# Kernel optimization log

Measured on AMD Instinct MI355X. Metric: run time of the kernel, lower is better.

Reference implementation:

```python
import jax, jax.numpy as jnp
import numpy as np

K = 9          # top-k neighbors
GROUPS = 4     # GroupNorm groups
EPS_GN = 1e-5  # torch GroupNorm default eps


def group_norm(x, gamma, beta):
    # x: [B, C, H, W]; normalize over (C/GROUPS, H, W) per group
    B, C, H, W = x.shape
    xg = x.reshape(B, GROUPS, -1)
    mu = xg.mean(axis=-1, keepdims=True)
    var = xg.var(axis=-1, keepdims=True)
    xn = ((xg - mu) / jnp.sqrt(var + EPS_GN)).reshape(B, C, H, W)
    return xn * gamma[None, :, None, None] + beta[None, :, None, None]


def setup_inputs() -> dict:
    key = jax.random.key(0)
    ks = jax.random.split(key, 6)
    B, C, H, W = 32, 128, 45, 45
    std = 1.0 / np.sqrt(C)
    x = jax.random.normal(ks[0], (B, C, H, W), dtype=jnp.float32)
    w1 = jax.random.uniform(ks[1], (C, C), jnp.float32, -std, std)
    b1 = jax.random.uniform(ks[2], (C,), jnp.float32, -std, std)
    w2 = jax.random.uniform(ks[3], (C, C), jnp.float32, -std, std)
    b2 = jax.random.uniform(ks[4], (C,), jnp.float32, -std, std)
    gamma1 = jnp.ones((C,), jnp.float32)
    beta1 = jnp.zeros((C,), jnp.float32)
    gamma2 = jnp.ones((C,), jnp.float32)
    beta2 = jnp.zeros((C,), jnp.float32)
    return {"x": x, "w1": w1, "b1": b1, "w2": w2, "b2": b2,
            "gamma1": gamma1, "beta1": beta1, "gamma2": gamma2, "beta2": beta2}


def reference(x, w1, b1, w2, b2, gamma1, beta1, gamma2, beta2):
    B, C, H, W = x.shape
    N = H * W
    # build_knn: flatten, L2-normalize, cosine sim, top-k
    xf = x.reshape(B, C, N).transpose(0, 2, 1)                  # [B, N, C]
    nrm = jnp.linalg.norm(xf, axis=-1, keepdims=True)
    xn = xf / jnp.maximum(nrm, 1e-12)                           # F.normalize
    sim = jnp.einsum('bnc,bmc->bnm', xn, xn)                    # [B, N, N]
    val, idx = jax.lax.top_k(sim, K)                            # [B, N, K]
    # normalized edge weights (shared by both GCN layers)
    v = val / (val.sum(axis=-1, keepdims=True) + 1e-6)          # [B, N, K]

    def gcn_apply(feat, w, b):
        xt = feat @ w                                           # [B, N, C]
        neigh = jax.vmap(lambda t, i: t[i])(xt, idx)            # [B, N, K, C]
        return jnp.einsum('bnkc,bnk->bnc', neigh, v) + b

    out = gcn_apply(xn, w1, b1)
    out = jax.nn.silu(group_norm(out.transpose(0, 2, 1).reshape(B, C, H, W), gamma1, beta1))
    of = out.reshape(B, C, N).transpose(0, 2, 1)
    out = gcn_apply(of, w2, b2)
    out = jax.nn.silu(group_norm(out.transpose(0, 2, 1).reshape(B, C, H, W), gamma2, beta2))
    return out
```

## Files before the change

kernel.cpp:

```cpp
#include <hip/hip_runtime.h>
#include <hip/hip_bf16.h>

#define BN 32
#define CC 128
#define NN 2025
#define KK 9
#define NGROUP 4
#define CPG 32
#define GN_EPS 1e-5f
#define ROWS_TOTAL (BN * NN)

typedef _Float16 f16;
typedef __attribute__((ext_vector_type(8))) _Float16 f16x8;
typedef __attribute__((ext_vector_type(4))) float f32x4;

#define S28 3.725290298461914e-09f
#define S40 9.094947017729282e-13f
#define RH  6.103515625e-05f
#define RL  1.4901161193847656e-08f

#define T0F 0.17f
#define CAP 100

__global__ __launch_bounds__(256) void k_normalize(const float* __restrict__ x,
                                                   f16* __restrict__ xh, f16* __restrict__ xl) {
    __shared__ float tile[128][65];
    const int b  = blockIdx.y;
    const int n0 = blockIdx.x * 64;
    const int t  = threadIdx.x;
    const int w  = t >> 6;
    const int lane = t & 63;
    const int gn_ld = min(n0 + lane, NN - 1);

    for (int it = 0; it < 32; ++it) {
        int c = it * 4 + w;
        tile[c][lane] = x[((size_t)(b * CC + c)) * NN + gn_ld];
    }
    __syncthreads();

    for (int i = 0; i < 16; ++i) {
        int n  = w * 16 + i;
        int gn = n0 + n;
        if (gn < NN) {
            float v0 = tile[lane][n];
            float v1 = tile[lane + 64][n];
            float ss = v0 * v0 + v1 * v1;
#pragma unroll
            for (int off = 32; off > 0; off >>= 1) ss += __shfl_xor(ss, off);
            float s = 1.0f / fmaxf(sqrtf(ss), 1e-12f);
            v0 *= s; v1 *= s;
            float w0 = v0 * 16384.0f, w1 = v1 * 16384.0f;
            f16 h0 = (f16)w0, h1 = (f16)w1;
            f16 l0 = (f16)((w0 - (float)h0) * 4096.0f);
            f16 l1 = (f16)((w1 - (float)h1) * 4096.0f);
            size_t base = (size_t)(b * NN + gn) * CC;
            xh[base + lane] = h0;  xh[base + lane + 64] = h1;
            xl[base + lane] = l0;  xl[base + lane + 64] = l1;
        }
    }
}

__device__ __forceinline__ void ins9(float cand, int m, float* v, int* ix,
                                     float& mv, int& mi, int& mp) {
    bool take = (cand > mv) || ((cand == mv) && (m < mi));
    if (take) {
#pragma unroll
        for (int k = 0; k < 9; ++k) if (k == mp) { v[k] = cand; ix[k] = m; }
        float nv = v[0]; int ni = ix[0]; int np = 0;
#pragma unroll
        for (int k = 1; k < 9; ++k) {
            if (v[k] < nv || (v[k] == nv && ix[k] > ni)) { nv = v[k]; ni = ix[k]; np = k; }
        }
        mv = nv; mi = ni; mp = np;
    }
}

__global__ __launch_bounds__(256) void k_sim_topk(const f16* __restrict__ xh, const f16* __restrict__ xl,
                                                  float* __restrict__ vout, int* __restrict__ iout) {
    __shared__ f16x8          stg[2][32][16];
    __shared__ float          sv[32][CAP + 1];
    __shared__ unsigned short si[32][CAP + 2];
    __shared__ int   cnt[32];
    __shared__ int   nbad;
    __shared__ int   badrows[32];

    const int id   = blockIdx.x;
    const int b    = (id & 7) + 8 * (id >> 9);
    const int r0   = ((id >> 3) & 63) * 32;
    const int t    = threadIdx.x;
    const int w    = t >> 6;
    const int lane = t & 63;
    const int jr   = lane & 15;
    const int q    = lane >> 4;
    const int tw   = w & 1;
    const int mh   = w >> 1;

    if (t < 32) cnt[t] = 0;
    if (t == 0) nbad = 0;

    f16x8 bh[4], bl[4];
    {
        int rr = b * NN + min(r0 + tw * 16 + jr, NN - 1);
        const f16* pH = xh + (size_t)rr * CC;
        const f16* pL = xl + (size_t)rr * CC;
#pragma unroll
        for (int s = 0; s < 4; ++s) {
            bh[s] = *(const f16x8*)(pH + s * 32 + q * 8);
            bl[s] = *(const f16x8*)(pL + s * 32 + q * 8);
        }
    }

    const int fi_ = t & 15;
    const int ri_ = t >> 4;
    const int fx  = fi_ ^ (ri_ & 7);
    const int rbuf = tw * 16 + jr;

    f16x8 h0r, h1r, l0r, l1r;
    {
        size_t g0 = (size_t)(b * NN + min(ri_, NN - 1)) * CC + fi_ * 8;
        size_t g1 = (size_t)(b * NN + min(ri_ + 16, NN - 1)) * CC + fi_ * 8;
        h0r = *(const f16x8*)(xh + g0);  h1r = *(const f16x8*)(xh + g1);
        l0r = *(const f16x8*)(xl + g0);  l1r = *(const f16x8*)(xl + g1);
    }

    for (int chunk = 0; chunk < 64; ++chunk) {
        __syncthreads();
        stg[0][ri_][fx]      = h0r;
        stg[0][ri_ + 16][fx] = h1r;
        stg[1][ri_][fx]      = l0r;
        stg[1][ri_ + 16][fx] = l1r;
        __syncthreads();
        if (chunk < 63) {
            size_t g0 = (size_t)(b * NN + min((chunk + 1) * 32 + ri_, NN - 1)) * CC + fi_ * 8;
            size_t g1 = (size_t)(b * NN + min((chunk + 1) * 32 + ri_ + 16, NN - 1)) * CC + fi_ * 8;
            h0r = *(const f16x8*)(xh + g0);  h1r = *(const f16x8*)(xh + g1);
            l0r = *(const f16x8*)(xl + g0);  l1r = *(const f16x8*)(xl + g1);
        }
        __builtin_amdgcn_sched_barrier(0);

        const int mb   = chunk * 32 + mh * 16;
        const int arow = mh * 16 + jr;
        const int axr  = arow & 7;
        f32x4 hh = {0.f, 0.f, 0.f, 0.f}, ll = {0.f, 0.f, 0.f, 0.f};
#pragma unroll
        for (int s = 0; s < 4; ++s) {
            f16x8 ah = stg[0][arow][(s * 4 + q) ^ axr];
            f16x8 al = stg[1][arow][(s * 4 + q) ^ axr];
            hh = __builtin_amdgcn_mfma_f32_16x16x32_f16(ah, bh[s], hh, 0, 0, 0);
            ll = __builtin_amdgcn_mfma_f32_16x16x32_f16(ah, bl[s], ll, 0, 0, 0);
            ll = __builtin_amdgcn_mfma_f32_16x16x32_f16(al, bh[s], ll, 0, 0, 0);
        }
#pragma unroll
        for (int reg = 0; reg < 4; ++reg) {
            int m = mb + q * 4 + reg;
            float c0 = hh[reg] * S28 + ll[reg] * S40;
            if (m < NN && c0 > T0F) {
                int pos = atomicAdd(&cnt[rbuf], 1);
                if (pos < CAP) { sv[rbuf][pos] = c0; si[rbuf][pos] = (unsigned short)m; }
            }
        }
    }
    __syncthreads();

    if (t < 32) {
        int r = r0 + t;
        if (r < NN) {
            int c = cnt[t];
            if (c >= 9 && c <= CAP) {
                float fv[9]; int fi[9];
#pragma unroll
                for (int k = 0; k < 9; ++k) { fv[k] = -3.0e38f; fi[k] = 0x7fffffff; }
                float mv = -3.0e38f; int mi = 0x7fffffff; int mp = 0;
                for (int j = 0; j < c; ++j) ins9(sv[t][j], (int)si[t][j], fv, fi, mv, mi, mp);
                float s = 1e-6f;
#pragma unroll
                for (int k = 0; k < 9; ++k) s += fv[k];
                float inv = 1.0f / s;
                int base = (b * NN + r) * KK;
#pragma unroll
                for (int k = 0; k < 9; ++k) { vout[base + k] = fv[k] * inv; iout[base + k] = fi[k]; }
            } else {
                int slot = atomicAdd(&nbad, 1);
                badrows[slot] = r;
            }
        }
    }
    __syncthreads();

    if (w == 0) {
        int nb = nbad;
        for (int ib = 0; ib < nb; ++ib) {
            int r = badrows[ib];
            const f16* rH = xh + ((size_t)b * NN + r) * CC;
            const f16* rL = xl + ((size_t)b * NN + r) * CC;
            float fv[9]; int fi[9];
#pragma unroll
            for (int k = 0; k < 9; ++k) { fv[k] = -3.0e38f; fi[k] = 0x7fffffff; }
            float mv = -3.0e38f; int mi = 0x7fffffff; int mp = 0;
            for (int m = lane; m < NN; m += 64) {
                const f16* mH = xh + ((size_t)b * NN + m) * CC;
                const f16* mL = xl + ((size_t)b * NN + m) * CC;
                float a1 = 0.f, a2 = 0.f;
                for (int c2 = 0; c2 < CC; ++c2) {
                    float hr = (float)rH[c2], hm = (float)mH[c2];
                    float lr = (float)rL[c2], lm = (float)mL[c2];
                    a1 += hr * hm;
                    a2 += hr * lm + lr * hm;
                }
                ins9(a1 * S28 + a2 * S40, m, fv, fi, mv, mi, mp);
            }
#pragma unroll
            for (int off = 1; off < 64; off <<= 1) {
                float pv[9]; int pi[9];
#pragma unroll
                for (int k = 0; k < 9; ++k) { pv[k] = __shfl_xor(fv[k], off); pi[k] = __shfl_xor(fi[k], off); }
#pragma unroll
                for (int k = 0; k < 9; ++k) ins9(pv[k], pi[k], fv, fi, mv, mi, mp);
            }
            if (lane == 0) {
                float s = 1e-6f;
#pragma unroll
                for (int k = 0; k < 9; ++k) s += fv[k];
                float inv = 1.0f / s;
                int base = (b * NN + r) * KK;
#pragma unroll
                for (int k = 0; k < 9; ++k) { vout[base + k] = fv[k] * inv; iout[base + k] = fi[k]; }
            }
        }
    }
}

#define RST 36
__global__ __launch_bounds__(256) void k_gemm_hl(const f16* __restrict__ xh, const f16* __restrict__ xl,
                                                 const float* __restrict__ w, float* __restrict__ out) {
    __shared__ float rowsT[CC * RST];
    int t = threadIdx.x;
    int row0 = blockIdx.x * 32;
    for (int it = 0; it < 16; ++it) {
        int qq = t + it * 256;
        int c = qq & 127, r = qq >> 7;
        size_t idx = (size_t)(row0 + r) * CC + c;
        rowsT[c * RST + r] = (float)xh[idx] * RH + (float)xl[idx] * RL;
    }
    __syncthreads();
    int j = t & 127, half = t >> 7;
    float acc[16];
#pragma unroll
    for (int r = 0; r < 16; ++r) acc[r] = 0.0f;
    for (int c = 0; c < CC; ++c) {
        float wv = w[c * CC + j];
        const float4* ap = (const float4*)&rowsT[c * RST + half * 16];
        float4 a0 = ap[0], a1 = ap[1], a2 = ap[2], a3 = ap[3];
        acc[0]  += a0.x * wv; acc[1]  += a0.y * wv; acc[2]  += a0.z * wv; acc[3]  += a0.w * wv;
        acc[4]  += a1.x * wv; acc[5]  += a1.y * wv; acc[6]  += a1.z * wv; acc[7]  += a1.w * wv;
        acc[8]  += a2.x * wv; acc[9]  += a2.y * wv; acc[10] += a2.z * wv; acc[11] += a2.w * wv;
        acc[12] += a3.x * wv; acc[13] += a3.y * wv; acc[14] += a3.z * wv; acc[15] += a3.w * wv;
    }
#pragma unroll
    for (int r = 0; r < 16; ++r) out[(size_t)(row0 + half * 16 + r) * CC + j] = acc[r];
}

__global__ __launch_bounds__(256) void k_gemm(const float* __restrict__ in,
                                              const float* __restrict__ w,
                                              float* __restrict__ out) {
    __shared__ float rowsT[CC * RST];
    int t = threadIdx.x;
    int row0 = blockIdx.x * 32;
    for (int it = 0; it < 16; ++it) {
        int qq = t + it * 256;
        int c = qq & 127, r = qq >> 7;
        rowsT[c * RST + r] = in[(size_t)(row0 + r) * CC + c];
    }
    __syncthreads();
    int j = t & 127, half = t >> 7;
    float acc[16];
#pragma unroll
    for (int r = 0; r < 16; ++r) acc[r] = 0.0f;
    for (int c = 0; c < CC; ++c) {
        float wv = w[c * CC + j];
        const float4* ap = (const float4*)&rowsT[c * RST + half * 16];
        float4 a0 = ap[0], a1 = ap[1], a2 = ap[2], a3 = ap[3];
        acc[0]  += a0.x * wv; acc[1]  += a0.y * wv; acc[2]  += a0.z * wv; acc[3]  += a0.w * wv;
        acc[4]  += a1.x * wv; acc[5]  += a1.y * wv; acc[6]  += a1.z * wv; acc[7]  += a1.w * wv;
        acc[8]  += a2.x * wv; acc[9]  += a2.y * wv; acc[10] += a2.z * wv; acc[11] += a2.w * wv;
        acc[12] += a3.x * wv; acc[13] += a3.y * wv; acc[14] += a3.z * wv; acc[15] += a3.w * wv;
    }
#pragma unroll
    for (int r = 0; r < 16; ++r) out[(size_t)(row0 + half * 16 + r) * CC + j] = acc[r];
}

__global__ __launch_bounds__(256) void k_gather(const float* __restrict__ xt,
                                                const float* __restrict__ v,
                                                const int* __restrict__ idx,
                                                const float* __restrict__ bias,
                                                float* __restrict__ out) {
    int t = threadIdx.x;
    int g = blockIdx.x * 2 + (t >> 7);
    int c = t & 127;
    if (g >= ROWS_TOTAL) return;
    int b = g / NN;
    int nb = b * NN;
    float acc = bias[c];
    int base = g * KK;
#pragma unroll
    for (int k = 0; k < KK; ++k) {
        int   ii = idx[base + k];
        float vv = v[base + k];
        acc += vv * xt[(size_t)(nb + ii) * CC + c];
    }
    out[(size_t)g * CC + c] = acc;
}

__global__ __launch_bounds__(256) void k_gnstats(const float* __restrict__ xin,
                                                 float* __restrict__ stats) {
    int bg = blockIdx.x; int b = bg >> 2; int gg = bg & 3;
    size_t base = (size_t)b * (NN * CC) + gg * CPG;
    float s1 = 0.f, s2 = 0.f;
    for (int i = threadIdx.x; i < NN * CPG; i += 256) {
        float x = xin[base + (size_t)(i >> 5) * CC + (i & 31)];
        s1 += x; s2 += x * x;
    }
#pragma unroll
    for (int off = 32; off > 0; off >>= 1) { s1 += __shfl_xor(s1, off); s2 += __shfl_xor(s2, off); }
    __shared__ float r1[4], r2[4];
    int w = threadIdx.x >> 6;
    if ((threadIdx.x & 63) == 0) { r1[w] = s1; r2[w] = s2; }
    __syncthreads();
    if (threadIdx.x == 0) {
        float a = r1[0] + r1[1] + r1[2] + r1[3];
        float qq = r2[0] + r2[1] + r2[2] + r2[3];
        const float inv = 1.0f / (float)(NN * CPG);
        float mean = a * inv;
        float var = qq * inv - mean * mean;
        stats[bg * 2]     = mean;
        stats[bg * 2 + 1] = rsqrtf(fmaxf(var, 0.f) + GN_EPS);
    }
}

__global__ __launch_bounds__(256) void k_gnsilu(const float* __restrict__ xin,
                                                const float* __restrict__ stats,
                                                const float* __restrict__ gamma,
                                                const float* __restrict__ beta,
                                                float* __restrict__ out) {
    size_t e4 = ((size_t)blockIdx.x * 256 + threadIdx.x) * 4;
    int c0 = (int)(e4 & 127);
    int b  = (int)(e4 / (NN * CC));
    int gg = c0 >> 5;
    float mean = stats[(b * 4 + gg) * 2];
    float rstd = stats[(b * 4 + gg) * 2 + 1];
    float4 x = *(const float4*)&xin[e4];
    float g0 = gamma[c0], g1 = gamma[c0 + 1], g2 = gamma[c0 + 2], g3 = gamma[c0 + 3];
    float p0 = beta[c0],  p1 = beta[c0 + 1],  p2 = beta[c0 + 2],  p3 = beta[c0 + 3];
    float y0 = (x.x - mean) * rstd * g0 + p0;
    float y1 = (x.y - mean) * rstd * g1 + p1;
    float y2 = (x.z - mean) * rstd * g2 + p2;
    float y3 = (x.w - mean) * rstd * g3 + p3;
    float4 r;
    r.x = y0 / (1.0f + expf(-y0));
    r.y = y1 / (1.0f + expf(-y1));
    r.z = y2 / (1.0f + expf(-y2));
    r.w = y3 / (1.0f + expf(-y3));
    *(float4*)&out[e4] = r;
}

__global__ __launch_bounds__(256) void k_gnsilu_out(const float* __restrict__ xin,
                                                    const float* __restrict__ stats,
                                                    const float* __restrict__ gamma,
                                                    const float* __restrict__ beta,
                                                    float* __restrict__ out) {
    __shared__ float tile[32 * 65];
    int b = blockIdx.z, ct = blockIdx.y, nt = blockIdx.x;
    int c0 = ct * 32, n0 = nt * 64;
    int t = threadIdx.x;
    int cj = t & 31, ni0 = t >> 5;
    int gg = c0 >> 5;
    float mean = stats[(b * 4 + gg) * 2];
    float rstd = stats[(b * 4 + gg) * 2 + 1];
    float gm = gamma[c0 + cj];
    float bt = beta[c0 + cj];
#pragma unroll
    for (int i = 0; i < 8; ++i) {
        int n = n0 + ni0 + i * 8;
        if (n < NN) {
            float x = xin[((size_t)b * NN + n) * CC + c0 + cj];
            float y = (x - mean) * rstd * gm + bt;
            y = y / (1.0f + expf(-y));
            tile[cj * 65 + ni0 + i * 8] = y;
        }
    }
    __syncthreads();
    int nj = t & 63, ci0 = t >> 6;
#pragma unroll
    for (int i = 0; i < 8; ++i) {
        int c = ci0 + i * 4;
        int n = n0 + nj;
        if (n < NN) out[((size_t)b * CC + c0 + c) * NN + n] = tile[c * 65 + nj];
    }
}

extern "C" void kernel_launch(void* const* d_in, const int* in_sizes, int n_in,
                              void* d_out, int out_size, void* d_ws, size_t ws_size,
                              hipStream_t stream) {
    const float* x      = (const float*)d_in[0];
    const float* w1     = (const float*)d_in[1];
    const float* b1     = (const float*)d_in[2];
    const float* w2     = (const float*)d_in[3];
    const float* b2     = (const float*)d_in[4];
    const float* gamma1 = (const float*)d_in[5];
    const float* beta1  = (const float*)d_in[6];
    const float* gamma2 = (const float*)d_in[7];
    const float* beta2  = (const float*)d_in[8];
    float* out = (float*)d_out;

    const size_t BIG = (size_t)ROWS_TOTAL * CC;
    float* ws   = (float*)d_ws;
    float* bufB = ws;
    f16*   xh   = (f16*)(ws + BIG);
    f16*   xl   = xh + BIG;
    float* bufA = ws + BIG;
    float* vbuf = ws + 2 * BIG;
    int*   ibuf = (int*)(ws + 2 * BIG + (size_t)ROWS_TOTAL * KK);
    float* stats = ws + 2 * BIG + 2 * (size_t)ROWS_TOTAL * KK;

    k_normalize<<<dim3(32, BN), 256, 0, stream>>>(x, xh, xl);
    k_sim_topk<<<2048, 256, 0, stream>>>(xh, xl, vbuf, ibuf);

    k_gemm_hl<<<(ROWS_TOTAL + 31) / 32, 256, 0, stream>>>(xh, xl, w1, bufB);
    k_gather<<<ROWS_TOTAL / 2, 256, 0, stream>>>(bufB, vbuf, ibuf, b1, bufA);
    k_gnstats<<<BN * NGROUP, 256, 0, stream>>>(bufA, stats);
    k_gnsilu<<<(int)(BIG / 1024), 256, 0, stream>>>(bufA, stats, gamma1, beta1, bufB);

    k_gemm<<<(ROWS_TOTAL + 31) / 32, 256, 0, stream>>>(bufB, w2, bufA);
    k_gather<<<ROWS_TOTAL / 2, 256, 0, stream>>>(bufA, vbuf, ibuf, b2, bufB);
    k_gnstats<<<BN * NGROUP, 256, 0, stream>>>(bufB, stats);
    k_gnsilu_out<<<dim3((NN + 63) / 64, NGROUP, BN), 256, 0, stream>>>(bufB, stats, gamma2, beta2, out);
}
```

Measured before the change: 659.6 us.

## Replace FP32 feature GEMMs with split-FP16 MFMA GEMMs and 16-bit neighbor indices

Both 128x128 feature projections now run on MFMA 16x16x32 f16 instructions. Operands are split into high and low f16 parts, with three products per tile to keep close to FP32 accuracy. Weights are pre-split and transposed by a small kernel, and the first GroupNorm+SiLU pass now writes split f16 activations directly instead of FP32. Neighbor indices are stored as 16-bit values, which cuts index traffic in the gather. The cost is extra MFMA work for the hi/lo cross terms and some precision risk from the fixed scaling factors.

After: 671.6 us. No clear change (+1.8%).

```diff
diff --git a/kernel.cpp b/kernel.cpp
--- a/kernel.cpp
+++ b/kernel.cpp
@@ -12,10 +12,13 @@
 
 typedef _Float16 f16;
 typedef __attribute__((ext_vector_type(8))) _Float16 f16x8;
+typedef __attribute__((ext_vector_type(4))) _Float16 f16x4;
 typedef __attribute__((ext_vector_type(4))) float f32x4;
 
 #define S28 3.725290298461914e-09f
 #define S40 9.094947017729282e-13f
+#define S26 1.4901161193847656e-08f
+#define S38 3.637978807091713e-12f
 #define RH  6.103515625e-05f
 #define RL  1.4901161193847656e-08f
 
@@ -76,7 +79,7 @@
 }
 
 __global__ __launch_bounds__(256) void k_sim_topk(const f16* __restrict__ xh, const f16* __restrict__ xl,
-                                                  float* __restrict__ vout, int* __restrict__ iout) {
+                                                  float* __restrict__ vout, unsigned short* __restrict__ iout) {
     __shared__ f16x8          stg[2][32][16];
     __shared__ float          sv[32][CAP + 1];
     __shared__ unsigned short si[32][CAP + 2];
@@ -178,7 +181,7 @@
                 float inv = 1.0f / s;
                 int base = (b * NN + r) * KK;
 #pragma unroll
-                for (int k = 0; k < 9; ++k) { vout[base + k] = fv[k] * inv; iout[base + k] = fi[k]; }
+                for (int k = 0; k < 9; ++k) { vout[base + k] = fv[k] * inv; iout[base + k] = (unsigned short)fi[k]; }
             } else {
                 int slot = atomicAdd(&nbad, 1);
                 badrows[slot] = r;
@@ -224,74 +227,86 @@
                 float inv = 1.0f / s;
                 int base = (b * NN + r) * KK;
 #pragma unroll
-                for (int k = 0; k < 9; ++k) { vout[base + k] = fv[k] * inv; iout[base + k] = fi[k]; }
+                for (int k = 0; k < 9; ++k) { vout[base + k] = fv[k] * inv; iout[base + k] = (unsigned short)fi[k]; }
             }
         }
     }
 }
 
-#define RST 36
-__global__ __launch_bounds__(256) void k_gemm_hl(const f16* __restrict__ xh, const f16* __restrict__ xl,
-                                                 const float* __restrict__ w, float* __restrict__ out) {
-    __shared__ float rowsT[CC * RST];
-    int t = threadIdx.x;
-    int row0 = blockIdx.x * 32;
-    for (int it = 0; it < 16; ++it) {
-        int qq = t + it * 256;
-        int c = qq & 127, r = qq >> 7;
-        size_t idx = (size_t)(row0 + r) * CC + c;
-        rowsT[c * RST + r] = (float)xh[idx] * RH + (float)xl[idx] * RL;
-    }
-    __syncthreads();
-    int j = t & 127, half = t >> 7;
-    float acc[16];
-#pragma unroll
-    for (int r = 0; r < 16; ++r) acc[r] = 0.0f;
-    for (int c = 0; c < CC; ++c) {
-        float wv = w[c * CC + j];
-        const float4* ap = (const float4*)&rowsT[c * RST + half * 16];
-        float4 a0 = ap[0], a1 = ap[1], a2 = ap[2], a3 = ap[3];
-        acc[0]  += a0.x * wv; acc[1]  += a0.y * wv; acc[2]  += a0.z * wv; acc[3]  += a0.w * wv;
-        acc[4]  += a1.x * wv; acc[5]  += a1.y * wv; acc[6]  += a1.z * wv; acc[7]  += a1.w * wv;
-        acc[8]  += a2.x * wv; acc[9]  += a2.y * wv; acc[10] += a2.z * wv; acc[11] += a2.w * wv;
-        acc[12] += a3.x * wv; acc[13] += a3.y * wv; acc[14] += a3.z * wv; acc[15] += a3.w * wv;
-    }
-#pragma unroll
-    for (int r = 0; r < 16; ++r) out[(size_t)(row0 + half * 16 + r) * CC + j] = acc[r];
-}
-
-__global__ __launch_bounds__(256) void k_gemm(const float* __restrict__ in,
-                                              const float* __restrict__ w,
-                                              float* __restrict__ out) {
-    __shared__ float rowsT[CC * RST];
-    int t = threadIdx.x;
-    int row0 = blockIdx.x * 32;
-    for (int it = 0; it < 16; ++it) {
-        int qq = t + it * 256;
-        int c = qq & 127, r = qq >> 7;
-        rowsT[c * RST + r] = in[(size_t)(row0 + r) * CC + c];
-    }
-    __syncthreads();
-    int j = t & 127, half = t >> 7;
-    float acc[16];
-#pragma unroll
-    for (int r = 0; r < 16; ++r) acc[r] = 0.0f;
-    for (int c = 0; c < CC; ++c) {
-        float wv = w[c * CC + j];
-        const float4* ap = (const float4*)&rowsT[c * RST + half * 16];
-        float4 a0 = ap[0], a1 = ap[1], a2 = ap[2], a3 = ap[3];
-        acc[0]  += a0.x * wv; acc[1]  += a0.y * wv; acc[2]  += a0.z * wv; acc[3]  += a0.w * wv;
-        acc[4]  += a1.x * wv; acc[5]  += a1.y * wv; acc[6]  += a1.z * wv; acc[7]  += a1.w * wv;
-        acc[8]  += a2.x * wv; acc[9]  += a2.y * wv; acc[10] += a2.z * wv; acc[11] += a2.w * wv;
-        acc[12] += a3.x * wv; acc[13] += a3.y * wv; acc[14] += a3.z * wv; acc[15] += a3.w * wv;
-    }
-#pragma unroll
-    for (int r = 0; r < 16; ++r) out[(size_t)(row0 + half * 16 + r) * CC + j] = acc[r];
+__global__ __launch_bounds__(256) void k_wsplit(const float* __restrict__ w1, const float* __restrict__ w2,
+                                                f16* __restrict__ wth1, f16* __restrict__ wtl1,
+                                                f16* __restrict__ wth2, f16* __restrict__ wtl2) {
+    const float* w = blockIdx.x ? w2 : w1;
+    f16* th = blockIdx.x ? wth2 : wth1;
+    f16* tl = blockIdx.x ? wtl2 : wtl1;
+    for (int e = threadIdx.x; e < CC * CC; e += 256) {
+        int c = e >> 7, j = e & 127;
+        float ws_ = w[e] * 16384.0f;
+        f16 h = (f16)ws_;
+        f16 l = (f16)((ws_ - (float)h) * 4096.0f);
+        th[j * CC + c] = h;
+        tl[j * CC + c] = l;
+    }
+}
+
+__global__ __launch_bounds__(256) void k_gemm_mf(const f16* __restrict__ ah, const f16* __restrict__ al,
+                                                 const f16* __restrict__ wth, const f16* __restrict__ wtl,
+                                                 float sH, float sL, float* __restrict__ out) {
+    const int t    = threadIdx.x;
+    const int w    = t >> 6;
+    const int lane = t & 63;
+    const int jr   = lane & 15;
+    const int q    = lane >> 4;
+    const int row0 = blockIdx.x * 32;
+
+    f16x8 wbh[2][4], wbl[2][4];
+#pragma unroll
+    for (int ct = 0; ct < 2; ++ct) {
+        int j = w * 32 + ct * 16 + jr;
+        const f16* pH = wth + (size_t)j * CC;
+        const f16* pL = wtl + (size_t)j * CC;
+#pragma unroll
+        for (int s = 0; s < 4; ++s) {
+            wbh[ct][s] = *(const f16x8*)(pH + s * 32 + q * 8);
+            wbl[ct][s] = *(const f16x8*)(pL + s * 32 + q * 8);
+        }
+    }
+
+#pragma unroll
+    for (int rt = 0; rt < 2; ++rt) {
+        int arow = row0 + rt * 16 + jr;
+        const f16* pA  = ah + (size_t)arow * CC;
+        const f16* pAl = al + (size_t)arow * CC;
+        f16x8 af[4], alf[4];
+#pragma unroll
+        for (int s = 0; s < 4; ++s) {
+            af[s]  = *(const f16x8*)(pA  + s * 32 + q * 8);
+            alf[s] = *(const f16x8*)(pAl + s * 32 + q * 8);
+        }
+        f32x4 hh0 = {0.f,0.f,0.f,0.f}, ll0 = {0.f,0.f,0.f,0.f};
+        f32x4 hh1 = {0.f,0.f,0.f,0.f}, ll1 = {0.f,0.f,0.f,0.f};
+#pragma unroll
+        for (int s = 0; s < 4; ++s) {
+            hh0 = __builtin_amdgcn_mfma_f32_16x16x32_f16(af[s],  wbh[0][s], hh0, 0, 0, 0);
+            ll0 = __builtin_amdgcn_mfma_f32_16x16x32_f16(af[s],  wbl[0][s], ll0, 0, 0, 0);
+            ll0 = __builtin_amdgcn_mfma_f32_16x16x32_f16(alf[s], wbh[0][s], ll0, 0, 0, 0);
+            hh1 = __builtin_amdgcn_mfma_f32_16x16x32_f16(af[s],  wbh[1][s], hh1, 0, 0, 0);
+            ll1 = __builtin_amdgcn_mfma_f32_16x16x32_f16(af[s],  wbl[1][s], ll1, 0, 0, 0);
+            ll1 = __builtin_amdgcn_mfma_f32_16x16x32_f16(alf[s], wbh[1][s], ll1, 0, 0, 0);
+        }
+#pragma unroll
+        for (int reg = 0; reg < 4; ++reg) {
+            int orow = row0 + rt * 16 + q * 4 + reg;
+            size_t ob = (size_t)orow * CC + w * 32 + jr;
+            out[ob]      = hh0[reg] * sH + ll0[reg] * sL;
+            out[ob + 16] = hh1[reg] * sH + ll1[reg] * sL;
+        }
+    }
 }
 
 __global__ __launch_bounds__(256) void k_gather(const float* __restrict__ xt,
                                                 const float* __restrict__ v,
-                                                const int* __restrict__ idx,
+                                                const unsigned short* __restrict__ idx,
                                                 const float* __restrict__ bias,
                                                 float* __restrict__ out) {
     int t = threadIdx.x;
@@ -304,7 +319,7 @@
     int base = g * KK;
 #pragma unroll
     for (int k = 0; k < KK; ++k) {
-        int   ii = idx[base + k];
+        int   ii = (int)idx[base + k];
         float vv = v[base + k];
         acc += vv * xt[(size_t)(nb + ii) * CC + c];
     }
@@ -337,11 +352,11 @@
     }
 }
 
-__global__ __launch_bounds__(256) void k_gnsilu(const float* __restrict__ xin,
-                                                const float* __restrict__ stats,
-                                                const float* __restrict__ gamma,
-                                                const float* __restrict__ beta,
-                                                float* __restrict__ out) {
+__global__ __launch_bounds__(256) void k_gnsilu_split(const float* __restrict__ xin,
+                                                      const float* __restrict__ stats,
+                                                      const float* __restrict__ gamma,
+                                                      const float* __restrict__ beta,
+                                                      f16* __restrict__ vh, f16* __restrict__ vl) {
     size_t e4 = ((size_t)blockIdx.x * 256 + threadIdx.x) * 4;
     int c0 = (int)(e4 & 127);
     int b  = (int)(e4 / (NN * CC));
@@ -355,12 +370,17 @@
     float y1 = (x.y - mean) * rstd * g1 + p1;
     float y2 = (x.z - mean) * rstd * g2 + p2;
     float y3 = (x.w - mean) * rstd * g3 + p3;
-    float4 r;
-    r.x = y0 / (1.0f + expf(-y0));
-    r.y = y1 / (1.0f + expf(-y1));
-    r.z = y2 / (1.0f + expf(-y2));
-    r.w = y3 / (1.0f + expf(-y3));
-    *(float4*)&out[e4] = r;
+    float r0 = y0 / (1.0f + expf(-y0));
+    float r1 = y1 / (1.0f + expf(-y1));
+    float r2 = y2 / (1.0f + expf(-y2));
+    float r3 = y3 / (1.0f + expf(-y3));
+    f16x4 hv, lv;
+    float s0 = r0 * 4096.0f; hv[0] = (f16)s0; lv[0] = (f16)((s0 - (float)hv[0]) * 4096.0f);
+    float s1 = r1 * 4096.0f; hv[1] = (f16)s1; lv[1] = (f16)((s1 - (float)hv[1]) * 4096.0f);
+    float s2 = r2 * 4096.0f; hv[2] = (f16)s2; lv[2] = (f16)((s2 - (float)hv[2]) * 4096.0f);
+    float s3 = r3 * 4096.0f; hv[3] = (f16)s3; lv[3] = (f16)((s3 - (float)hv[3]) * 4096.0f);
+    *(f16x4*)&vh[e4] = hv;
+    *(f16x4*)&vl[e4] = lv;
 }
 
 __global__ __launch_bounds__(256) void k_gnsilu_out(const float* __restrict__ xin,
@@ -413,24 +433,32 @@
     float* out = (float*)d_out;
 
     const size_t BIG = (size_t)ROWS_TOTAL * CC;
+    const size_t RK  = (size_t)ROWS_TOTAL * KK;
     float* ws   = (float*)d_ws;
     float* bufB = ws;
     f16*   xh   = (f16*)(ws + BIG);
     f16*   xl   = xh + BIG;
     float* bufA = ws + BIG;
     float* vbuf = ws + 2 * BIG;
-    int*   ibuf = (int*)(ws + 2 * BIG + (size_t)ROWS_TOTAL * KK);
-    float* stats = ws + 2 * BIG + 2 * (size_t)ROWS_TOTAL * KK;
+    unsigned short* ibuf = (unsigned short*)(ws + 2 * BIG + RK);
+    f16*   wth1 = (f16*)(ws + 2 * BIG + RK + RK / 2);
+    f16*   wtl1 = wth1 + CC * CC;
+    f16*   wth2 = wtl1 + CC * CC;
+    f16*   wtl2 = wth2 + CC * CC;
+    float* stats = ws + 2 * BIG + RK + RK / 2 + 2 * CC * CC;
+    f16*   vh = (f16*)bufB;
+    f16*   vl = vh + BIG;
 
     k_normalize<<<dim3(32, BN), 256, 0, stream>>>(x, xh, xl);
+    k_wsplit<<<2, 256, 0, stream>>>(w1, w2, wth1, wtl1, wth2, wtl2);
     k_sim_topk<<<2048, 256, 0, stream>>>(xh, xl, vbuf, ibuf);
 
-    k_gemm_hl<<<(ROWS_TOTAL + 31) / 32, 256, 0, stream>>>(xh, xl, w1, bufB);
+    k_gemm_mf<<<ROWS_TOTAL / 32, 256, 0, stream>>>(xh, xl, wth1, wtl1, S28, S40, bufB);
     k_gather<<<ROWS_TOTAL / 2, 256, 0, stream>>>(bufB, vbuf, ibuf, b1, bufA);
     k_gnstats<<<BN * NGROUP, 256, 0, stream>>>(bufA, stats);
-    k_gnsilu<<<(int)(BIG / 1024), 256, 0, stream>>>(bufA, stats, gamma1, beta1, bufB);
-
-    k_gemm<<<(ROWS_TOTAL + 31) / 32, 256, 0, stream>>>(bufB, w2, bufA);
+    k_gnsilu_split<<<(int)(BIG / 1024), 256, 0, stream>>>(bufA, stats, gamma1, beta1, vh, vl);
+
+    k_gemm_mf<<<ROWS_TOTAL / 32, 256, 0, stream>>>(vh, vl, wth2, wtl2, S26, S38, bufA);
     k_gather<<<ROWS_TOTAL / 2, 256, 0, stream>>>(bufA, vbuf, ibuf, b2, bufB);
     k_gnstats<<<BN * NGROUP, 256, 0, stream>>>(bufB, stats);
     k_gnsilu_out<<<dim3((NN + 63) / 64, NGROUP, BN), 256, 0, stream>>>(bufB, stats, gamma2, beta2, out);
```
